# Kernel optimization log

Measured on AMD Instinct MI355X. Metric: run time of the kernel, lower is better.

Reference implementation:

```python
import jax, jax.numpy as jnp
import numpy as np
from jax import lax

EPS = 1e-5
NBIT = 127.0  # 8-bit symmetric: 2^(8-1)-1

def ste_round(x):
    return x + lax.stop_gradient(jnp.round(x) - x)

def quant_act(x, rng_max):
    # symmetric fake-quant of activations with learned per-cluster range
    s = rng_max / NBIT
    xq = jnp.clip(ste_round(x / s), -NBIT, NBIT) * s
    return xq, s

def fold_bn(w, gamma, beta, mean, var):
    std = jnp.sqrt(var + EPS)
    scale = gamma / std
    w_f = w * scale[:, None, None, None]
    b_f = beta - mean * scale
    return w_f, b_f

def quant_weight(w):
    # per-output-channel symmetric quant
    s = jnp.max(jnp.abs(w), axis=(1, 2, 3), keepdims=True) / NBIT
    wq = jnp.clip(ste_round(w / s), -NBIT, NBIT) * s
    return wq, s.reshape(-1)

def conv(x, w, stride=1, groups=1, pad=0):
    return lax.conv_general_dilated(
        x, w, window_strides=(stride, stride),
        padding=((pad, pad), (pad, pad)),
        dimension_numbers=('NCHW', 'OIHW', 'NCHW'),
        feature_group_count=groups)

def setup_inputs() -> dict:
    key = jax.random.key(0)
    ks = jax.random.split(key, 24)
    B, Cin, H, W = 64, 96, 28, 28
    Cmid, Cout, NC = 576, 96, 4
    d = {}
    d['x'] = jax.random.normal(ks[0], (B, Cin, H, W), dtype=jnp.float32)
    # conv1: 1x1 expansion
    d['w1'] = jax.random.normal(ks[1], (Cmid, Cin, 1, 1), jnp.float32) * 0.1
    d['g1'] = jax.random.uniform(ks[2], (Cmid,), minval=0.5, maxval=1.5)
    d['b1'] = jax.random.normal(ks[3], (Cmid,)) * 0.1
    d['m1'] = jax.random.normal(ks[4], (Cmid,)) * 0.1
    d['v1'] = jax.random.uniform(ks[5], (Cmid,), minval=0.5, maxval=1.5)
    # conv2: 3x3 depthwise
    d['w2'] = jax.random.normal(ks[6], (Cmid, 1, 3, 3), jnp.float32) * 0.1
    d['g2'] = jax.random.uniform(ks[7], (Cmid,), minval=0.5, maxval=1.5)
    d['b2'] = jax.random.normal(ks[8], (Cmid,)) * 0.1
    d['m2'] = jax.random.normal(ks[9], (Cmid,)) * 0.1
    d['v2'] = jax.random.uniform(ks[10], (Cmid,), minval=0.5, maxval=1.5)
    # conv3: 1x1 projection
    d['w3'] = jax.random.normal(ks[11], (Cout, Cmid, 1, 1), jnp.float32) * 0.1
    d['g3'] = jax.random.uniform(ks[12], (Cout,), minval=0.5, maxval=1.5)
    d['b3'] = jax.random.normal(ks[13], (Cout,)) * 0.1
    d['m3'] = jax.random.normal(ks[14], (Cout,)) * 0.1
    d['v3'] = jax.random.uniform(ks[15], (Cout,), minval=0.5, maxval=1.5)
    # per-cluster learned activation ranges for the 4 QuantAct modules
    d['r0'] = jax.random.uniform(ks[16], (NC,), minval=2.0, maxval=8.0)
    d['r1'] = jax.random.uniform(ks[17], (NC,), minval=2.0, maxval=8.0)
    d['r2'] = jax.random.uniform(ks[18], (NC,), minval=2.0, maxval=8.0)
    d['r3'] = jax.random.uniform(ks[19], (NC,), minval=2.0, maxval=8.0)
    d['cluster'] = 2
    return d

def reference(x, w1, g1, b1, m1, v1, w2, g2, b2, m2, v2,
              w3, g3, b3, m3, v3, r0, r1, r2, r3, cluster):
    identity = x  # residual path (in==out, stride==1)
    # QuantAct -> conv1 (BN-folded, per-channel quant) -> ReLU6
    xq, s0 = quant_act(x, r0[cluster])
    w1f, bf1 = fold_bn(w1, g1, b1, m1, v1)
    w1q, ws1 = quant_weight(w1f)
    y = conv(xq, w1q) + bf1[None, :, None, None]
    y = jnp.clip(y, 0.0, 6.0)
    # QuantAct1 -> depthwise conv2 -> ReLU6
    yq, s1 = quant_act(y, r1[cluster])
    w2f, bf2 = fold_bn(w2, g2, b2, m2, v2)
    w2q, ws2 = quant_weight(w2f)
    y = conv(yq, w2q, stride=1, groups=w2.shape[0], pad=1) + bf2[None, :, None, None]
    y = jnp.clip(y, 0.0, 6.0)
    # QuantAct2 -> conv3 projection
    yq, s2 = quant_act(y, r2[cluster])
    w3f, bf3 = fold_bn(w3, g3, b3, m3, v3)
    w3q, ws3 = quant_weight(w3f)
    y = conv(yq, w3q) + bf3[None, :, None, None]
    # residual add, then int32 requant
    y = y + identity
    out, s3 = quant_act(y, r3[cluster])
    return out, s3
```

## Files before the change

### kernel.cpp

```cpp
#include <hip/hip_runtime.h>
#include <cstdint>
#include <cstddef>

typedef int   v4i __attribute__((ext_vector_type(4)));
typedef float v4f __attribute__((ext_vector_type(4)));
typedef unsigned int u32;

constexpr int B_   = 64;
constexpr int CIN  = 96;
constexpr int P_   = 784;
constexpr int CMID = 576;
constexpr int COUT = 96;
constexpr int NOUT = B_ * COUT * P_;
constexpr float NBITF = 127.0f;
constexpr float EPSF  = 1e-5f;
constexpr float MAGICF = 12582912.0f;
constexpr int   BIASI  = 0x4B400000;

constexpr int XB4 = 13 * 8 * 64;
constexpr int YB4 = 13 * 36 * 64;

__device__ __forceinline__ int dot3(u32 a, u32 w, int acc) {
#if __has_builtin(__builtin_amdgcn_sdot4)
    return __builtin_amdgcn_sdot4((int)a, (int)w, acc, false);
#else
    return acc + (int)(signed char)(a)        * (int)(signed char)(w)
               + (int)(signed char)(a >> 8)   * (int)(signed char)(w >> 8)
               + (int)(signed char)(a >> 16)  * (int)(signed char)(w >> 16);
#endif
}

__device__ __forceinline__ void tr4(u32 S0, u32 S1, u32 S2, u32 S3, u32 O[4]) {
    u32 u01 = __builtin_amdgcn_perm(S1, S0, 0x05010400u);
    u32 u23 = __builtin_amdgcn_perm(S3, S2, 0x05010400u);
    u32 v01 = __builtin_amdgcn_perm(S1, S0, 0x07030602u);
    u32 v23 = __builtin_amdgcn_perm(S3, S2, 0x07030602u);
    O[0] = __builtin_amdgcn_perm(u23, u01, 0x05040100u);
    O[1] = __builtin_amdgcn_perm(u23, u01, 0x07060302u);
    O[2] = __builtin_amdgcn_perm(v23, v01, 0x05040100u);
    O[3] = __builtin_amdgcn_perm(v23, v01, 0x07060302u);
}

__device__ __forceinline__ u32 pack4(u32 t0, u32 t1, u32 t2, u32 t3) {
    u32 p01 = __builtin_amdgcn_perm(t1, t0, 0x05010400u);
    u32 p23 = __builtin_amdgcn_perm(t3, t2, 0x05010400u);
    return __builtin_amdgcn_perm(p23, p01, 0x05040100u);
}

__global__ __launch_bounds__(256)
void prep_all(const float* __restrict__ x,
              const float* __restrict__ w1, const float* __restrict__ g1,
              const float* __restrict__ b1, const float* __restrict__ m1,
              const float* __restrict__ v1,
              const float* __restrict__ w2, const float* __restrict__ g2,
              const float* __restrict__ b2, const float* __restrict__ m2,
              const float* __restrict__ v2,
              const float* __restrict__ w3, const float* __restrict__ g3,
              const float* __restrict__ b3, const float* __restrict__ m3,
              const float* __restrict__ v3,
              const float* __restrict__ r0, const int* __restrict__ cluster,
              u32* __restrict__ x8t2,
              int8_t* __restrict__ w1qp, float* __restrict__ ws1, float* __restrict__ bf1,
              v4i* __restrict__ w2pk, float* __restrict__ ws2, float* __restrict__ bf2,
              int8_t* __restrict__ w3qp, float* __restrict__ ws3, float* __restrict__ bf3)
{
    __shared__ u32 T[112 * 37];
    int tid = threadIdx.x;

    if (blockIdx.x < 448) {
        int pt0 = blockIdx.x % 7, b = blockIdx.x / 7;
        float inv_s0 = NBITF / r0[cluster[0]];

        for (int i = tid; i < 112 * 8; i += 256) {
            int row = i >> 3, c = 24 + (i & 7);
            T[row * 37 + c] = 0u;
        }
        for (int u = tid; u < 24 * 28; u += 256) {
            int pq = u % 28, icq = u / 28;
            int pxb = pt0 * 112 + pq * 4;
            int q[4][4];
            #pragma unroll
            for (int j = 0; j < 4; j++) {
                v4f xv = *(const v4f*)(x + ((size_t)b * CIN + icq * 4 + j) * P_ + pxb);
                #pragma unroll
                for (int i = 0; i < 4; i++)
                    q[j][i] = (int)fminf(fmaxf(rintf(xv[i] * inv_s0), -127.f), 127.f);
            }
            #pragma unroll
            for (int i = 0; i < 4; i++) {
                u32 t0 = __builtin_amdgcn_perm((u32)q[1][i], (u32)q[0][i], 0x00000400u);
                u32 t1 = __builtin_amdgcn_perm((u32)q[3][i], (u32)q[2][i], 0x00000400u);
                T[(pq * 4 + i) * 37 + icq] = __builtin_amdgcn_perm(t1, t0, 0x05040100u);
            }
        }
        __syncthreads();
        u32* gb = x8t2 + (size_t)b * XB4 * 4;
        for (int i = tid; i < 32 * 112; i += 256) {
            int icq = i / 112, pxo = i - icq * 112;
            int px = pt0 * 112 + pxo;
            gb[(((px >> 6) * 8 + (icq >> 2)) * 64 + (px & 63)) * 4 + (icq & 3)] =
                T[pxo * 37 + icq];
        }
        return;
    }

    int lane = tid & 63, wv = tid >> 6;
    int blk = (blockIdx.x - 448) * 4 + wv;

    const float *w, *g, *bb, *mm, *vv;
    int oc, K, which;
    if (blk < CMID)            { which = 0; w = w1; g = g1; bb = b1; mm = m1; vv = v1; oc = blk;            K = CIN;  }
    else if (blk < 2 * CMID)   { which = 1; w = w2; g = g2; bb = b2; mm = m2; vv = v2; oc = blk - CMID;     K = 9;    }
    else                       { which = 2; w = w3; g = g3; bb = b3; mm = m3; vv = v3; oc = blk - 2 * CMID; K = CMID; }

    float scale = g[oc] / sqrtf(vv[oc] + EPSF);

    float mx = 0.f;
    for (int k = lane; k < K; k += 64)
        mx = fmaxf(mx, fabsf(w[oc * K + k] * scale));
    #pragma unroll
    for (int off = 1; off < 64; off <<= 1)
        mx = fmaxf(mx, __shfl_xor(mx, off));

    float s = mx / NBITF;

    int myq = 0;
    for (int k = lane; k < K; k += 64) {
        float wf = w[oc * K + k] * scale;
        float q  = fminf(fmaxf(rintf(wf / s), -127.f), 127.f);
        if (which == 0)      w1qp[oc * 144 + k] = (int8_t)q;
        else if (which == 1) myq = (int)q;
        else                 w3qp[oc * 592 + k] = (int8_t)q;
    }
    if (which == 0 && lane < 12)
        ((u32*)(w1qp + oc * 144))[24 + lane] = 0u;
    if (which == 1) {
        u32 qq[9];
        #pragma unroll
        for (int t = 0; t < 9; t++) qq[t] = (u32)__shfl(myq, t, 64) & 0xffu;
        if (lane == 0) {
            v4i pk;
            pk[0] = (int)(qq[0] | (qq[1] << 8) | (qq[2] << 16));
            pk[1] = (int)(qq[3] | (qq[4] << 8) | (qq[5] << 16));
            pk[2] = (int)(qq[6] | (qq[7] << 8) | (qq[8] << 16));
            pk[3] = 0;
            w2pk[oc] = pk;
        }
    }
    if (lane == 0) {
        float bf = bb[oc] - mm[oc] * scale;
        if (which == 0)      { ws1[oc] = s; bf1[oc] = bf; }
        else if (which == 1) { ws2[oc] = s; bf2[oc] = bf; }
        else                 { ws3[oc] = s; bf3[oc] = bf; }
    }
}

__global__ __launch_bounds__(256)
void conv12r(const u32* __restrict__ x8t2, const int8_t* __restrict__ w1qp,
             const float* __restrict__ ws1, const float* __restrict__ bf1,
             const v4i* __restrict__ w2pk, const float* __restrict__ ws2,
             const float* __restrict__ bf2,
             const float* __restrict__ r0, const float* __restrict__ r1,
             const float* __restrict__ r2, const int* __restrict__ cluster,
             v4i* __restrict__ y2t)
{
    __shared__ u32 y1w[192 * 29];
    __shared__ u32 y2s[192 * 15];

    int tid = threadIdx.x, b = blockIdx.y;
    int mt = blockIdx.x / 14, rt = blockIdx.x - mt * 14;
    int R0 = 2 * rt;
    int W0 = (R0 - 1) * 28;
    int lane = tid & 63, wv = tid >> 6;
    int n = lane & 15, q4 = lane >> 4;
    int ocw = mt * 192 + wv * 48;

    int   c      = cluster[0];
    float s0     = r0[c] / NBITF;
    float s1     = r1[c] / NBITF;
    float inv_s1 = NBITF / r1[c];
    float inv_s2 = NBITF / r2[c];
    int   u1i    = (int)fminf(rintf(6.f * inv_s1), 127.f);
    int   u2i    = (int)fminf(rintf(6.f * inv_s2), 127.f);

    const v4i* xb = (const v4i*)x8t2 + (size_t)b * XB4;
    int pb[7];
    #pragma unroll
    for (int jm = 0; jm < 7; jm++) {
        int px = W0 + 16 * jm + n;
        px = min(max(px, 0), P_ - 1);
        pb[jm] = (px >> 6) * 512 + (px & 63);
    }

    v4i acc[3][7];
    #pragma unroll
    for (int jn = 0; jn < 3; jn++)
        #pragma unroll
        for (int jm = 0; jm < 7; jm++) acc[jn][jm] = (v4i){0, 0, 0, 0};

    const v4i* w4 = (const v4i*)w1qp;
    #pragma unroll
    for (int ks = 0; ks < 2; ks++) {
        v4i bw[3];
        #pragma unroll
        for (int jn = 0; jn < 3; jn++)
            bw[jn] = w4[(ocw + 16 * jn + n) * 9 + 4 * ks + q4];
        int go = (4 * ks + q4) * 64;
        #pragma unroll
        for (int jm = 0; jm < 7; jm++) {
            v4i af = xb[pb[jm] + go];
            #pragma unroll
            for (int jn = 0; jn < 3; jn++)
                acc[jn][jm] = __builtin_amdgcn_mfma_i32_16x16x64_i8(af, bw[jn], acc[jn][jm], 0, 0, 0);
        }
    }

    #pragma unroll
    for (int jn = 0; jn < 3; jn++) {
        int   oc  = ocw + 16 * jn + n;
        int   chl = wv * 48 + 16 * jn + n;
        float scv = s0 * ws1[oc] * inv_s1;
        float bbv = bf1[oc] * inv_s1;
        #pragma unroll
        for (int jm = 0; jm < 7; jm++) {
            u32 t[4];
            #pragma unroll
            for (int r = 0; r < 4; r++) {
                float f = fmaf((float)acc[jn][jm][r], scv, bbv) + MAGICF;
                t[r] = (u32)min(max(__float_as_int(f), BIASI), BIASI + u1i);
            }
            int dw = 4 * jm + q4;
            u32 pk = pack4(t[0], t[1], t[2], t[3]);
            pk = ((unsigned)(W0 + 4 * dw) < (unsigned)P_) ? pk : 0u;
            y1w[chl * 29 + dw] = pk;
        }
    }
    __syncthreads();

    for (int u = tid; u < 384; u += 256) {
        int chl = u >> 1, orow = u & 1;
        int ch  = mt * 192 + chl;
        int rb  = chl * 29 + orow * 7;

        v4i wpk = w2pk[ch];
        u32 pk0 = (u32)wpk[0], pk1 = (u32)wpk[1], pk2 = (u32)wpk[2];
        float scv = s1 * ws2[ch] * inv_s2;
        float bbv = bf2[ch] * inv_s2;

        u32 M0 = 0, M1 = 0, M2 = 0;
        u32 D0 = y1w[rb], D1 = y1w[rb + 7], D2 = y1w[rb + 14];
        #pragma unroll
        for (int xq = 0; xq < 7; xq++) {
            u32 N0, N1, N2;
            if (xq < 6) {
                N0 = y1w[rb + xq + 1];
                N1 = y1w[rb + 7 + xq + 1];
                N2 = y1w[rb + 14 + xq + 1];
            } else { N0 = N1 = N2 = 0u; }

            int a0, a1, a2, a3;
            a0 = dot3(__builtin_amdgcn_alignbyte(D0, M0, 3), pk0, 0);
            a0 = dot3(__builtin_amdgcn_alignbyte(D1, M1, 3), pk1, a0);
            a0 = dot3(__builtin_amdgcn_alignbyte(D2, M2, 3), pk2, a0);
            a1 = dot3(D0, pk0, 0);
            a1 = dot3(D1, pk1, a1);
            a1 = dot3(D2, pk2, a1);
            a2 = dot3(__builtin_amdgcn_alignbyte(N0, D0, 1), pk0, 0);
            a2 = dot3(__builtin_amdgcn_alignbyte(N1, D1, 1), pk1, a2);
            a2 = dot3(__builtin_amdgcn_alignbyte(N2, D2, 1), pk2, a2);
            a3 = dot3(__builtin_amdgcn_alignbyte(N0, D0, 2), pk0, 0);
            a3 = dot3(__builtin_amdgcn_alignbyte(N1, D1, 2), pk1, a3);
            a3 = dot3(__builtin_amdgcn_alignbyte(N2, D2, 2), pk2, a3);

            int aa[4] = {a0, a1, a2, a3};
            u32 tq[4];
            #pragma unroll
            for (int i = 0; i < 4; i++) {
                float f = fmaf((float)aa[i], scv, bbv) + MAGICF;
                tq[i] = (u32)min(max(__float_as_int(f), BIASI), BIASI + u2i);
            }
            y2s[chl * 15 + orow * 7 + xq] = pack4(tq[0], tq[1], tq[2], tq[3]);

            M0 = D0; M1 = D1; M2 = D2;
            D0 = N0; D1 = N1; D2 = N2;
        }
    }
    __syncthreads();

    v4i* yb = y2t + (size_t)b * YB4;
    for (int u = tid; u < 168; u += 256) {
        int kgl = u / 14, d = u - kgl * 14;
        u32 O[4][4];
        #pragma unroll
        for (int j = 0; j < 4; j++) {
            int cb = (16 * kgl + 4 * j) * 15 + d;
            tr4(y2s[cb], y2s[cb + 15], y2s[cb + 30], y2s[cb + 45], O[j]);
        }
        int gpx0 = R0 * 28 + 4 * d;
        #pragma unroll
        for (int i = 0; i < 4; i++) {
            int gp = gpx0 + i;
            v4i val = (v4i){(int)O[0][i], (int)O[1][i], (int)O[2][i], (int)O[3][i]};
            yb[((gp >> 6) * 36 + mt * 12 + kgl) * 64 + (gp & 63)] = val;
        }
    }
}

__global__ __launch_bounds__(256)
void conv3d(const v4i* __restrict__ y2t, const int8_t* __restrict__ w3qp,
            const float* __restrict__ ws3, const float* __restrict__ bf3,
            const float* __restrict__ x, const float* __restrict__ r2,
            const float* __restrict__ r3, const int* __restrict__ cluster,
            float* __restrict__ out)
{
    int tid = threadIdx.x, b = blockIdx.y, pt = blockIdx.x;
    int lane = tid & 63, wv = tid >> 6;
    int n = lane & 15, q4 = lane >> 4;
    int pxl = wv * 16 + n;
    int px  = pt * 64 + pxl;
    int pxc = min(px, P_ - 1);

    int   c      = cluster[0];
    float s2     = r2[c] / NBITF;
    float s3     = r3[c] / NBITF;
    float inv_s3 = NBITF / r3[c];

    const v4i* yb  = y2t + (size_t)b * YB4;
    int pb3 = (pxc >> 6) * (36 * 64) + (pxc & 63);
    const v4i* w34 = (const v4i*)w3qp;

    v4i acc[6];
    #pragma unroll
    for (int i = 0; i < 6; i++) acc[i] = (v4i){0, 0, 0, 0};

    #pragma unroll
    for (int ks = 0; ks < 9; ks++) {
        v4i bfr = yb[pb3 + (4 * ks + q4) * 64];
        #pragma unroll
        for (int i = 0; i < 6; i++) {
            v4i afr = w34[(i * 16 + n) * 37 + 4 * ks + q4];
            acc[i] = __builtin_amdgcn_mfma_i32_16x16x64_i8(afr, bfr, acc[i], 0, 0, 0);
        }
    }

    if (px < P_) {
        #pragma unroll
        for (int i = 0; i < 6; i++) {
            #pragma unroll
            for (int r = 0; r < 4; r++) {
                int oc = i * 16 + q4 * 4 + r;
                size_t gi = (size_t)(b * COUT + oc) * P_ + px;
                float v  = (float)acc[i][r] * (s2 * ws3[oc]) + bf3[oc] + x[gi];
                float f  = fmaf(v, inv_s3, MAGICF);
                int lvl  = min(max(__float_as_int(f) - BIASI, -127), 127);
                out[gi]  = (float)lvl * s3;
            }
        }
    }
    if (pt == 0 && b == 0 && tid == 0)
        out[NOUT] = s3;
}

extern "C" void kernel_launch(void* const* d_in, const int* in_sizes, int n_in,
                              void* d_out, int out_size, void* d_ws, size_t ws_size,
                              hipStream_t stream)
{
    const float* x  = (const float*)d_in[0];
    const float* w1 = (const float*)d_in[1];
    const float* g1 = (const float*)d_in[2];
    const float* b1 = (const float*)d_in[3];
    const float* m1 = (const float*)d_in[4];
    const float* v1 = (const float*)d_in[5];
    const float* w2 = (const float*)d_in[6];
    const float* g2 = (const float*)d_in[7];
    const float* b2 = (const float*)d_in[8];
    const float* m2 = (const float*)d_in[9];
    const float* v2 = (const float*)d_in[10];
    const float* w3 = (const float*)d_in[11];
    const float* g3 = (const float*)d_in[12];
    const float* b3 = (const float*)d_in[13];
    const float* m3 = (const float*)d_in[14];
    const float* v3 = (const float*)d_in[15];
    const float* r0 = (const float*)d_in[16];
    const float* r1 = (const float*)d_in[17];
    const float* r2 = (const float*)d_in[18];
    const float* r3 = (const float*)d_in[19];
    const int*   cl = (const int*)d_in[20];

    float* out = (float*)d_out;

    char*  ws  = (char*)d_ws;
    size_t off = 0;
    auto carve = [&](size_t bytes) {
        size_t cur = off;
        off = (off + bytes + 255) & ~(size_t)255;
        return (void*)(ws + cur);
    };
    int8_t* w1qp = (int8_t*)carve((size_t)CMID * 144);
    float*  ws1  = (float*)carve(CMID * 4);
    float*  bf1  = (float*)carve(CMID * 4);
    v4i*    w2pk = (v4i*)carve((size_t)CMID * 16);
    float*  ws2  = (float*)carve(CMID * 4);
    float*  bf2  = (float*)carve(CMID * 4);
    int8_t* w3qp = (int8_t*)carve((size_t)COUT * 592);
    float*  ws3  = (float*)carve(COUT * 4);
    float*  bf3  = (float*)carve(COUT * 4);
    u32*    x8t2 = (u32*)carve((size_t)B_ * XB4 * 16);
    v4i*    y2t  = (v4i*)carve((size_t)B_ * YB4 * 16);
    (void)ws_size; (void)in_sizes; (void)n_in; (void)out_size;

    prep_all<<<dim3(760), dim3(256), 0, stream>>>(
        x, w1, g1, b1, m1, v1, w2, g2, b2, m2, v2, w3, g3, b3, m3, v3,
        r0, cl, x8t2,
        w1qp, ws1, bf1, w2pk, ws2, bf2, w3qp, ws3, bf3);

    conv12r<<<dim3(42, B_), dim3(256), 0, stream>>>(
        x8t2, w1qp, ws1, bf1, w2pk, ws2, bf2, r0, r1, r2, cl, y2t);

    conv3d<<<dim3(13, B_), dim3(256), 0, stream>>>(
        y2t, w3qp, ws3, bf3, x, r2, r3, cl, out);
}
```

Baseline: 177.6 us.

## Move depthwise conv into projection kernel, materialize conv1 output globally

The fusion boundary moves: conv1 now runs as its own kernel and writes quantized int8 activations to global memory, without recomputing halo rows. A new kernel reads those rows, does the depthwise 3x3 for all 576 channels per two-row tile, transposes in shared memory and runs the projection MFMA plus residual requant, so the y2 tensor never goes to global memory. Per-channel scale and bias are also pre-folded into float2 pairs during prep. The cost is a larger global intermediate for y1 (about 29 MB) and a big LDS footprint in the fused kernel, which may reduce occupancy.

```diff
diff --git a/kernel.cpp b/kernel.cpp
--- a/kernel.cpp
+++ b/kernel.cpp
@@ -18,7 +18,6 @@
 constexpr int   BIASI  = 0x4B400000;
 
 constexpr int XB4 = 13 * 8 * 64;
-constexpr int YB4 = 13 * 36 * 64;
 
 __device__ __forceinline__ int dot3(u32 a, u32 w, int acc) {
 #if __has_builtin(__builtin_amdgcn_sdot4)
@@ -58,22 +57,24 @@
               const float* __restrict__ w3, const float* __restrict__ g3,
               const float* __restrict__ b3, const float* __restrict__ m3,
               const float* __restrict__ v3,
-              const float* __restrict__ r0, const int* __restrict__ cluster,
+              const float* __restrict__ r0, const float* __restrict__ r1,
+              const float* __restrict__ r2, const int* __restrict__ cluster,
               u32* __restrict__ x8t2,
-              int8_t* __restrict__ w1qp, float* __restrict__ ws1, float* __restrict__ bf1,
-              v4i* __restrict__ w2pk, float* __restrict__ ws2, float* __restrict__ bf2,
-              int8_t* __restrict__ w3qp, float* __restrict__ ws3, float* __restrict__ bf3)
+              int8_t* __restrict__ w1qp, float2* __restrict__ e1,
+              v4i* __restrict__ w2pk,    float2* __restrict__ e2,
+              int8_t* __restrict__ w3qp, float2* __restrict__ e3)
 {
     __shared__ u32 T[112 * 37];
     int tid = threadIdx.x;
+    int c = cluster[0];
 
     if (blockIdx.x < 448) {
         int pt0 = blockIdx.x % 7, b = blockIdx.x / 7;
-        float inv_s0 = NBITF / r0[cluster[0]];
+        float inv_s0 = NBITF / r0[c];
 
         for (int i = tid; i < 112 * 8; i += 256) {
-            int row = i >> 3, c = 24 + (i & 7);
-            T[row * 37 + c] = 0u;
+            int row = i >> 3, cc = 24 + (i & 7);
+            T[row * 37 + cc] = 0u;
         }
         for (int u = tid; u < 24 * 28; u += 256) {
             int pq = u % 28, icq = u / 28;
@@ -149,66 +150,59 @@
     }
     if (lane == 0) {
         float bf = bb[oc] - mm[oc] * scale;
-        if (which == 0)      { ws1[oc] = s; bf1[oc] = bf; }
-        else if (which == 1) { ws2[oc] = s; bf2[oc] = bf; }
-        else                 { ws3[oc] = s; bf3[oc] = bf; }
+        float s0 = r0[c] / NBITF, s1 = r1[c] / NBITF, s2 = r2[c] / NBITF;
+        if (which == 0) {
+            float inv_s1 = NBITF / r1[c];
+            e1[oc] = make_float2(s0 * s * inv_s1, bf * inv_s1);
+        } else if (which == 1) {
+            float inv_s2 = NBITF / r2[c];
+            e2[oc] = make_float2(s1 * s * inv_s2, bf * inv_s2);
+        } else {
+            e3[oc] = make_float2(s2 * s, bf);
+        }
     }
 }
 
 __global__ __launch_bounds__(256)
-void conv12r(const u32* __restrict__ x8t2, const int8_t* __restrict__ w1qp,
-             const float* __restrict__ ws1, const float* __restrict__ bf1,
-             const v4i* __restrict__ w2pk, const float* __restrict__ ws2,
-             const float* __restrict__ bf2,
-             const float* __restrict__ r0, const float* __restrict__ r1,
-             const float* __restrict__ r2, const int* __restrict__ cluster,
-             v4i* __restrict__ y2t)
+void conv1f(const v4i* __restrict__ x8t2, const v4i* __restrict__ w1q4,
+            const float2* __restrict__ e1, const float* __restrict__ r1,
+            const int* __restrict__ cluster, u32* __restrict__ y1px)
 {
-    __shared__ u32 y1w[192 * 29];
-    __shared__ u32 y2s[192 * 15];
+    __shared__ u32 L[192 * 20];
 
     int tid = threadIdx.x, b = blockIdx.y;
-    int mt = blockIdx.x / 14, rt = blockIdx.x - mt * 14;
-    int R0 = 2 * rt;
-    int W0 = (R0 - 1) * 28;
+    int mt = blockIdx.x % 3, pt = blockIdx.x / 3;
+    int p0 = pt * 64;
     int lane = tid & 63, wv = tid >> 6;
     int n = lane & 15, q4 = lane >> 4;
     int ocw = mt * 192 + wv * 48;
 
-    int   c      = cluster[0];
-    float s0     = r0[c] / NBITF;
-    float s1     = r1[c] / NBITF;
-    float inv_s1 = NBITF / r1[c];
-    float inv_s2 = NBITF / r2[c];
-    int   u1i    = (int)fminf(rintf(6.f * inv_s1), 127.f);
-    int   u2i    = (int)fminf(rintf(6.f * inv_s2), 127.f);
-
-    const v4i* xb = (const v4i*)x8t2 + (size_t)b * XB4;
-    int pb[7];
-    #pragma unroll
-    for (int jm = 0; jm < 7; jm++) {
-        int px = W0 + 16 * jm + n;
-        px = min(max(px, 0), P_ - 1);
+    int u1i = (int)fminf(rintf(6.f * NBITF / r1[cluster[0]]), 127.f);
+
+    const v4i* xb = x8t2 + (size_t)b * XB4;
+    int pb[4];
+    #pragma unroll
+    for (int jm = 0; jm < 4; jm++) {
+        int px = min(p0 + 16 * jm + n, P_ - 1);
         pb[jm] = (px >> 6) * 512 + (px & 63);
     }
 
-    v4i acc[3][7];
+    v4i acc[3][4];
     #pragma unroll
     for (int jn = 0; jn < 3; jn++)
         #pragma unroll
-        for (int jm = 0; jm < 7; jm++) acc[jn][jm] = (v4i){0, 0, 0, 0};
-
-    const v4i* w4 = (const v4i*)w1qp;
+        for (int jm = 0; jm < 4; jm++) acc[jn][jm] = (v4i){0, 0, 0, 0};
+
     #pragma unroll
     for (int ks = 0; ks < 2; ks++) {
+        int g = 4 * ks + q4;
         v4i bw[3];
         #pragma unroll
         for (int jn = 0; jn < 3; jn++)
-            bw[jn] = w4[(ocw + 16 * jn + n) * 9 + 4 * ks + q4];
-        int go = (4 * ks + q4) * 64;
-        #pragma unroll
-        for (int jm = 0; jm < 7; jm++) {
-            v4i af = xb[pb[jm] + go];
+            bw[jn] = w1q4[(ocw + 16 * jn + n) * 9 + g];
+        #pragma unroll
+        for (int jm = 0; jm < 4; jm++) {
+            v4i af = xb[pb[jm] + g * 64];
             #pragma unroll
             for (int jn = 0; jn < 3; jn++)
                 acc[jn][jm] = __builtin_amdgcn_mfma_i32_16x16x64_i8(af, bw[jn], acc[jn][jm], 0, 0, 0);
@@ -217,116 +211,127 @@
 
     #pragma unroll
     for (int jn = 0; jn < 3; jn++) {
-        int   oc  = ocw + 16 * jn + n;
-        int   chl = wv * 48 + 16 * jn + n;
-        float scv = s0 * ws1[oc] * inv_s1;
-        float bbv = bf1[oc] * inv_s1;
-        #pragma unroll
-        for (int jm = 0; jm < 7; jm++) {
+        int    ocl = wv * 48 + 16 * jn + n;
+        float2 e   = e1[ocw + 16 * jn + n];
+        #pragma unroll
+        for (int jm = 0; jm < 4; jm++) {
             u32 t[4];
             #pragma unroll
             for (int r = 0; r < 4; r++) {
-                float f = fmaf((float)acc[jn][jm][r], scv, bbv) + MAGICF;
+                float f = fmaf((float)acc[jn][jm][r], e.x, e.y) + MAGICF;
                 t[r] = (u32)min(max(__float_as_int(f), BIASI), BIASI + u1i);
             }
-            int dw = 4 * jm + q4;
-            u32 pk = pack4(t[0], t[1], t[2], t[3]);
-            pk = ((unsigned)(W0 + 4 * dw) < (unsigned)P_) ? pk : 0u;
-            y1w[chl * 29 + dw] = pk;
+            L[ocl * 20 + 4 * jm + q4] = pack4(t[0], t[1], t[2], t[3]);
         }
     }
     __syncthreads();
 
-    for (int u = tid; u < 384; u += 256) {
-        int chl = u >> 1, orow = u & 1;
-        int ch  = mt * 192 + chl;
-        int rb  = chl * 29 + orow * 7;
-
+    for (int u = tid; u < 768; u += 256) {
+        int ocl = u >> 2, dq = u & 3;
+        int dwg = pt * 16 + 4 * dq;
+        if (dwg < 196) {
+            v4i val = *(const v4i*)&L[ocl * 20 + 4 * dq];
+            *(v4i*)&y1px[(size_t)(b * CMID + mt * 192 + ocl) * 196 + dwg] = val;
+        }
+    }
+}
+
+__global__ __launch_bounds__(256)
+void conv23f(const u32* __restrict__ y1px, const v4i* __restrict__ w2pk,
+             const float2* __restrict__ e2, const int8_t* __restrict__ w3qp,
+             const float2* __restrict__ e3, const float* __restrict__ x,
+             const float* __restrict__ r2, const float* __restrict__ r3,
+             const int* __restrict__ cluster, float* __restrict__ out)
+{
+    __shared__ u32 y2px[CMID * 15];
+    __shared__ v4i y2t[36 * 57];
+
+    int tid = threadIdx.x, b = blockIdx.y, rt = blockIdx.x;
+    int R0 = 2 * rt;
+
+    int   c      = cluster[0];
+    float inv_s3 = NBITF / r3[c];
+    float s3     = r3[c] / NBITF;
+    int   u2i    = (int)fminf(rintf(6.f * NBITF / r2[c]), 127.f);
+
+    for (int ch = tid; ch < CMID; ch += 256) {
+        const u32* base = y1px + (size_t)(b * CMID + ch) * 196;
+        u32 row[4][7];
+        #pragma unroll
+        for (int j = 0; j < 4; j++) {
+            int rr = R0 - 1 + j;
+            bool ok = (unsigned)rr < 28u;
+            #pragma unroll
+            for (int k = 0; k < 7; k++)
+                row[j][k] = ok ? base[rr * 7 + k] : 0u;
+        }
         v4i wpk = w2pk[ch];
         u32 pk0 = (u32)wpk[0], pk1 = (u32)wpk[1], pk2 = (u32)wpk[2];
-        float scv = s1 * ws2[ch] * inv_s2;
-        float bbv = bf2[ch] * inv_s2;
-
-        u32 M0 = 0, M1 = 0, M2 = 0;
-        u32 D0 = y1w[rb], D1 = y1w[rb + 7], D2 = y1w[rb + 14];
-        #pragma unroll
-        for (int xq = 0; xq < 7; xq++) {
-            u32 N0, N1, N2;
-            if (xq < 6) {
-                N0 = y1w[rb + xq + 1];
-                N1 = y1w[rb + 7 + xq + 1];
-                N2 = y1w[rb + 14 + xq + 1];
-            } else { N0 = N1 = N2 = 0u; }
-
-            int a0, a1, a2, a3;
-            a0 = dot3(__builtin_amdgcn_alignbyte(D0, M0, 3), pk0, 0);
-            a0 = dot3(__builtin_amdgcn_alignbyte(D1, M1, 3), pk1, a0);
-            a0 = dot3(__builtin_amdgcn_alignbyte(D2, M2, 3), pk2, a0);
-            a1 = dot3(D0, pk0, 0);
-            a1 = dot3(D1, pk1, a1);
-            a1 = dot3(D2, pk2, a1);
-            a2 = dot3(__builtin_amdgcn_alignbyte(N0, D0, 1), pk0, 0);
-            a2 = dot3(__builtin_amdgcn_alignbyte(N1, D1, 1), pk1, a2);
-            a2 = dot3(__builtin_amdgcn_alignbyte(N2, D2, 1), pk2, a2);
-            a3 = dot3(__builtin_amdgcn_alignbyte(N0, D0, 2), pk0, 0);
-            a3 = dot3(__builtin_amdgcn_alignbyte(N1, D1, 2), pk1, a3);
-            a3 = dot3(__builtin_amdgcn_alignbyte(N2, D2, 2), pk2, a3);
-
-            int aa[4] = {a0, a1, a2, a3};
-            u32 tq[4];
-            #pragma unroll
-            for (int i = 0; i < 4; i++) {
-                float f = fmaf((float)aa[i], scv, bbv) + MAGICF;
-                tq[i] = (u32)min(max(__float_as_int(f), BIASI), BIASI + u2i);
+        float2 e = e2[ch];
+
+        #pragma unroll
+        for (int orow = 0; orow < 2; orow++) {
+            u32 M0 = 0, M1 = 0, M2 = 0;
+            u32 D0 = row[orow][0], D1 = row[orow + 1][0], D2 = row[orow + 2][0];
+            #pragma unroll
+            for (int xq = 0; xq < 7; xq++) {
+                u32 N0, N1, N2;
+                if (xq < 6) {
+                    N0 = row[orow][xq + 1];
+                    N1 = row[orow + 1][xq + 1];
+                    N2 = row[orow + 2][xq + 1];
+                } else { N0 = N1 = N2 = 0u; }
+
+                int a0, a1, a2, a3;
+                a0 = dot3(__builtin_amdgcn_alignbyte(D0, M0, 3), pk0, 0);
+                a0 = dot3(__builtin_amdgcn_alignbyte(D1, M1, 3), pk1, a0);
+                a0 = dot3(__builtin_amdgcn_alignbyte(D2, M2, 3), pk2, a0);
+                a1 = dot3(D0, pk0, 0);
+                a1 = dot3(D1, pk1, a1);
+                a1 = dot3(D2, pk2, a1);
+                a2 = dot3(__builtin_amdgcn_alignbyte(N0, D0, 1), pk0, 0);
+                a2 = dot3(__builtin_amdgcn_alignbyte(N1, D1, 1), pk1, a2);
+                a2 = dot3(__builtin_amdgcn_alignbyte(N2, D2, 1), pk2, a2);
+                a3 = dot3(__builtin_amdgcn_alignbyte(N0, D0, 2), pk0, 0);
+                a3 = dot3(__builtin_amdgcn_alignbyte(N1, D1, 2), pk1, a3);
+                a3 = dot3(__builtin_amdgcn_alignbyte(N2, D2, 2), pk2, a3);
+
+                int aa[4] = {a0, a1, a2, a3};
+                u32 tq[4];
+                #pragma unroll
+                for (int i = 0; i < 4; i++) {
+                    float f = fmaf((float)aa[i], e.x, e.y) + MAGICF;
+                    tq[i] = (u32)min(max(__float_as_int(f), BIASI), BIASI + u2i);
+                }
+                y2px[ch * 15 + orow * 7 + xq] = pack4(tq[0], tq[1], tq[2], tq[3]);
+
+                M0 = D0; M1 = D1; M2 = D2;
+                D0 = N0; D1 = N1; D2 = N2;
             }
-            y2s[chl * 15 + orow * 7 + xq] = pack4(tq[0], tq[1], tq[2], tq[3]);
-
-            M0 = D0; M1 = D1; M2 = D2;
-            D0 = N0; D1 = N1; D2 = N2;
         }
     }
     __syncthreads();
 
-    v4i* yb = y2t + (size_t)b * YB4;
-    for (int u = tid; u < 168; u += 256) {
-        int kgl = u / 14, d = u - kgl * 14;
+    for (int u = tid; u < 504; u += 256) {
+        int kg = u / 14, d = u - kg * 14;
         u32 O[4][4];
         #pragma unroll
         for (int j = 0; j < 4; j++) {
-            int cb = (16 * kgl + 4 * j) * 15 + d;
-            tr4(y2s[cb], y2s[cb + 15], y2s[cb + 30], y2s[cb + 45], O[j]);
-        }
-        int gpx0 = R0 * 28 + 4 * d;
-        #pragma unroll
-        for (int i = 0; i < 4; i++) {
-            int gp = gpx0 + i;
-            v4i val = (v4i){(int)O[0][i], (int)O[1][i], (int)O[2][i], (int)O[3][i]};
-            yb[((gp >> 6) * 36 + mt * 12 + kgl) * 64 + (gp & 63)] = val;
-        }
-    }
-}
-
-__global__ __launch_bounds__(256)
-void conv3d(const v4i* __restrict__ y2t, const int8_t* __restrict__ w3qp,
-            const float* __restrict__ ws3, const float* __restrict__ bf3,
-            const float* __restrict__ x, const float* __restrict__ r2,
-            const float* __restrict__ r3, const int* __restrict__ cluster,
-            float* __restrict__ out)
-{
-    int tid = threadIdx.x, b = blockIdx.y, pt = blockIdx.x;
+            int cb = (16 * kg + 4 * j) * 15 + d;
+            tr4(y2px[cb], y2px[cb + 15], y2px[cb + 30], y2px[cb + 45], O[j]);
+        }
+        #pragma unroll
+        for (int i = 0; i < 4; i++)
+            y2t[kg * 57 + 4 * d + i] =
+                (v4i){(int)O[0][i], (int)O[1][i], (int)O[2][i], (int)O[3][i]};
+    }
+    __syncthreads();
+
     int lane = tid & 63, wv = tid >> 6;
     int n = lane & 15, q4 = lane >> 4;
     int pxl = wv * 16 + n;
-    int px  = pt * 64 + pxl;
-    int pxc = min(px, P_ - 1);
-
-    int   c      = cluster[0];
-    float s2     = r2[c] / NBITF;
-    float s3     = r3[c] / NBITF;
-    float inv_s3 = NBITF / r3[c];
-
-    const v4i* yb  = y2t + (size_t)b * YB4;
-    int pb3 = (pxc >> 6) * (36 * 64) + (pxc & 63);
+    int pxc = min(pxl, 55);
+
     const v4i* w34 = (const v4i*)w3qp;
 
     v4i acc[6];
@@ -335,7 +340,7 @@
 
     #pragma unroll
     for (int ks = 0; ks < 9; ks++) {
-        v4i bfr = yb[pb3 + (4 * ks + q4) * 64];
+        v4i bfr = y2t[(4 * ks + q4) * 57 + pxc];
         #pragma unroll
         for (int i = 0; i < 6; i++) {
             v4i afr = w34[(i * 16 + n) * 37 + 4 * ks + q4];
@@ -343,21 +348,23 @@
         }
     }
 
-    if (px < P_) {
+    if (pxl < 56) {
+        int px = R0 * 28 + pxl;
         #pragma unroll
         for (int i = 0; i < 6; i++) {
             #pragma unroll
             for (int r = 0; r < 4; r++) {
-                int oc = i * 16 + q4 * 4 + r;
+                int    oc = i * 16 + q4 * 4 + r;
+                float2 e  = e3[oc];
                 size_t gi = (size_t)(b * COUT + oc) * P_ + px;
-                float v  = (float)acc[i][r] * (s2 * ws3[oc]) + bf3[oc] + x[gi];
+                float v  = fmaf((float)acc[i][r], e.x, e.y) + x[gi];
                 float f  = fmaf(v, inv_s3, MAGICF);
                 int lvl  = min(max(__float_as_int(f) - BIASI, -127), 127);
                 out[gi]  = (float)lvl * s3;
             }
         }
     }
-    if (pt == 0 && b == 0 && tid == 0)
+    if (rt == 0 && b == 0 && tid == 0)
         out[NOUT] = s3;
 }
 
@@ -397,26 +404,23 @@
         return (void*)(ws + cur);
     };
     int8_t* w1qp = (int8_t*)carve((size_t)CMID * 144);
-    float*  ws1  = (float*)carve(CMID * 4);
-    float*  bf1  = (float*)carve(CMID * 4);
+    float2* e1   = (float2*)carve((size_t)CMID * 8);
     v4i*    w2pk = (v4i*)carve((size_t)CMID * 16);
-    float*  ws2  = (float*)carve(CMID * 4);
-    float*  bf2  = (float*)carve(CMID * 4);
+    float2* e2   = (float2*)carve((size_t)CMID * 8);
     int8_t* w3qp = (int8_t*)carve((size_t)COUT * 592);
-    float*  ws3  = (float*)carve(COUT * 4);
-    float*  bf3  = (float*)carve(COUT * 4);
+    float2* e3   = (float2*)carve((size_t)COUT * 8);
     u32*    x8t2 = (u32*)carve((size_t)B_ * XB4 * 16);
-    v4i*    y2t  = (v4i*)carve((size_t)B_ * YB4 * 16);
+    u32*    y1px = (u32*)carve((size_t)B_ * CMID * 196 * 4);
     (void)ws_size; (void)in_sizes; (void)n_in; (void)out_size;
 
     prep_all<<<dim3(760), dim3(256), 0, stream>>>(
         x, w1, g1, b1, m1, v1, w2, g2, b2, m2, v2, w3, g3, b3, m3, v3,
-        r0, cl, x8t2,
-        w1qp, ws1, bf1, w2pk, ws2, bf2, w3qp, ws3, bf3);
-
-    conv12r<<<dim3(42, B_), dim3(256), 0, stream>>>(
-        x8t2, w1qp, ws1, bf1, w2pk, ws2, bf2, r0, r1, r2, cl, y2t);
-
-    conv3d<<<dim3(13, B_), dim3(256), 0, stream>>>(
-        y2t, w3qp, ws3, bf3, x, r2, r3, cl, out);
-}
+        r0, r1, r2, cl, x8t2,
+        w1qp, e1, w2pk, e2, w3qp, e3);
+
+    conv1f<<<dim3(39, B_), dim3(256), 0, stream>>>(
+        (const v4i*)x8t2, (const v4i*)w1qp, e1, r1, cl, y1px);
+
+    conv23f<<<dim3(14, B_), dim3(256), 0, stream>>>(
+        y1px, w2pk, e2, w3qp, e3, x, r2, r3, cl, out);
+}
```

Result: slower. 199.2 us (+12.1%).

## Stage input tile in LDS for conv1 and precompute fused per-channel epilogue scales

Applied to the files above, without the earlier changes.

conv12 now loads the int8 input tile for its 112 pixels into shared memory once, instead of every wave reading the fragments from global memory, and the shared pool is reused afterward for the depthwise output. The jn loop is moved outside, so each wave keeps only 7 accumulators at a time rather than 21, which lowers register pressure. The requant scale and bias for each channel are now computed once in prep_all and stored as float2, so the conv kernels read one pair instead of recombining several scalars. The cost is an extra __syncthreads and an LDS staging pass at the start of conv12.

```diff
diff --git a/kernel.cpp b/kernel.cpp
--- a/kernel.cpp
+++ b/kernel.cpp
@@ -58,22 +58,24 @@
               const float* __restrict__ w3, const float* __restrict__ g3,
               const float* __restrict__ b3, const float* __restrict__ m3,
               const float* __restrict__ v3,
-              const float* __restrict__ r0, const int* __restrict__ cluster,
+              const float* __restrict__ r0, const float* __restrict__ r1,
+              const float* __restrict__ r2, const int* __restrict__ cluster,
               u32* __restrict__ x8t2,
-              int8_t* __restrict__ w1qp, float* __restrict__ ws1, float* __restrict__ bf1,
-              v4i* __restrict__ w2pk, float* __restrict__ ws2, float* __restrict__ bf2,
-              int8_t* __restrict__ w3qp, float* __restrict__ ws3, float* __restrict__ bf3)
+              int8_t* __restrict__ w1qp, float2* __restrict__ e1,
+              v4i* __restrict__ w2pk,    float2* __restrict__ e2,
+              int8_t* __restrict__ w3qp, float2* __restrict__ e3)
 {
     __shared__ u32 T[112 * 37];
     int tid = threadIdx.x;
+    int c = cluster[0];
 
     if (blockIdx.x < 448) {
         int pt0 = blockIdx.x % 7, b = blockIdx.x / 7;
-        float inv_s0 = NBITF / r0[cluster[0]];
+        float inv_s0 = NBITF / r0[c];
 
         for (int i = tid; i < 112 * 8; i += 256) {
-            int row = i >> 3, c = 24 + (i & 7);
-            T[row * 37 + c] = 0u;
+            int row = i >> 3, cc = 24 + (i & 7);
+            T[row * 37 + cc] = 0u;
         }
         for (int u = tid; u < 24 * 28; u += 256) {
             int pq = u % 28, icq = u / 28;
@@ -149,23 +151,28 @@
     }
     if (lane == 0) {
         float bf = bb[oc] - mm[oc] * scale;
-        if (which == 0)      { ws1[oc] = s; bf1[oc] = bf; }
-        else if (which == 1) { ws2[oc] = s; bf2[oc] = bf; }
-        else                 { ws3[oc] = s; bf3[oc] = bf; }
+        float s0 = r0[c] / NBITF, s1 = r1[c] / NBITF, s2 = r2[c] / NBITF;
+        if (which == 0) {
+            float inv_s1 = NBITF / r1[c];
+            e1[oc] = make_float2(s0 * s * inv_s1, bf * inv_s1);
+        } else if (which == 1) {
+            float inv_s2 = NBITF / r2[c];
+            e2[oc] = make_float2(s1 * s * inv_s2, bf * inv_s2);
+        } else {
+            e3[oc] = make_float2(s2 * s, bf);
+        }
     }
 }
 
 __global__ __launch_bounds__(256)
-void conv12r(const u32* __restrict__ x8t2, const int8_t* __restrict__ w1qp,
-             const float* __restrict__ ws1, const float* __restrict__ bf1,
-             const v4i* __restrict__ w2pk, const float* __restrict__ ws2,
-             const float* __restrict__ bf2,
-             const float* __restrict__ r0, const float* __restrict__ r1,
-             const float* __restrict__ r2, const int* __restrict__ cluster,
-             v4i* __restrict__ y2t)
+void conv12v3(const v4i* __restrict__ x8t2, const v4i* __restrict__ w1q4,
+              const float2* __restrict__ e1,
+              const v4i* __restrict__ w2pk, const float2* __restrict__ e2,
+              const float* __restrict__ r1, const float* __restrict__ r2,
+              const int* __restrict__ cluster, v4i* __restrict__ y2t)
 {
+    __shared__ u32 pool[112 * 36];
     __shared__ u32 y1w[192 * 29];
-    __shared__ u32 y2s[192 * 15];
 
     int tid = threadIdx.x, b = blockIdx.y;
     int mt = blockIdx.x / 14, rt = blockIdx.x - mt * 14;
@@ -175,58 +182,46 @@
     int n = lane & 15, q4 = lane >> 4;
     int ocw = mt * 192 + wv * 48;
 
-    int   c      = cluster[0];
-    float s0     = r0[c] / NBITF;
-    float s1     = r1[c] / NBITF;
-    float inv_s1 = NBITF / r1[c];
-    float inv_s2 = NBITF / r2[c];
-    int   u1i    = (int)fminf(rintf(6.f * inv_s1), 127.f);
-    int   u2i    = (int)fminf(rintf(6.f * inv_s2), 127.f);
-
-    const v4i* xb = (const v4i*)x8t2 + (size_t)b * XB4;
-    int pb[7];
-    #pragma unroll
-    for (int jm = 0; jm < 7; jm++) {
-        int px = W0 + 16 * jm + n;
-        px = min(max(px, 0), P_ - 1);
-        pb[jm] = (px >> 6) * 512 + (px & 63);
-    }
-
-    v4i acc[3][7];
-    #pragma unroll
-    for (int jn = 0; jn < 3; jn++)
-        #pragma unroll
-        for (int jm = 0; jm < 7; jm++) acc[jn][jm] = (v4i){0, 0, 0, 0};
-
-    const v4i* w4 = (const v4i*)w1qp;
-    #pragma unroll
-    for (int ks = 0; ks < 2; ks++) {
-        v4i bw[3];
-        #pragma unroll
-        for (int jn = 0; jn < 3; jn++)
-            bw[jn] = w4[(ocw + 16 * jn + n) * 9 + 4 * ks + q4];
-        int go = (4 * ks + q4) * 64;
-        #pragma unroll
-        for (int jm = 0; jm < 7; jm++) {
-            v4i af = xb[pb[jm] + go];
-            #pragma unroll
-            for (int jn = 0; jn < 3; jn++)
-                acc[jn][jm] = __builtin_amdgcn_mfma_i32_16x16x64_i8(af, bw[jn], acc[jn][jm], 0, 0, 0);
-        }
-    }
+    int c   = cluster[0];
+    int u1i = (int)fminf(rintf(6.f * NBITF / r1[c]), 127.f);
+    int u2i = (int)fminf(rintf(6.f * NBITF / r2[c]), 127.f);
+
+    const v4i* xb = x8t2 + (size_t)b * XB4;
+    for (int u = tid; u < 896; u += 256) {
+        int g = u / 112, pxl = u - g * 112;
+        int px = min(max(W0 + pxl, 0), P_ - 1);
+        v4i v = xb[((px >> 6) * 8 + g) * 64 + (px & 63)];
+        *(v4i*)&pool[pxl * 36 + 4 * g] = v;
+    }
+    __syncthreads();
 
     #pragma unroll
     for (int jn = 0; jn < 3; jn++) {
-        int   oc  = ocw + 16 * jn + n;
-        int   chl = wv * 48 + 16 * jn + n;
-        float scv = s0 * ws1[oc] * inv_s1;
-        float bbv = bf1[oc] * inv_s1;
+        int oc  = ocw + 16 * jn + n;
+        int chl = wv * 48 + 16 * jn + n;
+
+        v4i acc[7];
+        #pragma unroll
+        for (int jm = 0; jm < 7; jm++) acc[jm] = (v4i){0, 0, 0, 0};
+
+        #pragma unroll
+        for (int ks = 0; ks < 2; ks++) {
+            v4i bw = w1q4[oc * 9 + 4 * ks + q4];
+            int g4 = (4 * ks + q4) * 4;
+            #pragma unroll
+            for (int jm = 0; jm < 7; jm++) {
+                v4i af = *(const v4i*)&pool[(16 * jm + n) * 36 + g4];
+                acc[jm] = __builtin_amdgcn_mfma_i32_16x16x64_i8(af, bw, acc[jm], 0, 0, 0);
+            }
+        }
+
+        float2 e = e1[oc];
         #pragma unroll
         for (int jm = 0; jm < 7; jm++) {
             u32 t[4];
             #pragma unroll
             for (int r = 0; r < 4; r++) {
-                float f = fmaf((float)acc[jn][jm][r], scv, bbv) + MAGICF;
+                float f = fmaf((float)acc[jm][r], e.x, e.y) + MAGICF;
                 t[r] = (u32)min(max(__float_as_int(f), BIASI), BIASI + u1i);
             }
             int dw = 4 * jm + q4;
@@ -237,6 +232,7 @@
     }
     __syncthreads();
 
+    u32* y2s = pool;
     for (int u = tid; u < 384; u += 256) {
         int chl = u >> 1, orow = u & 1;
         int ch  = mt * 192 + chl;
@@ -244,8 +240,7 @@
 
         v4i wpk = w2pk[ch];
         u32 pk0 = (u32)wpk[0], pk1 = (u32)wpk[1], pk2 = (u32)wpk[2];
-        float scv = s1 * ws2[ch] * inv_s2;
-        float bbv = bf2[ch] * inv_s2;
+        float2 e = e2[ch];
 
         u32 M0 = 0, M1 = 0, M2 = 0;
         u32 D0 = y1w[rb], D1 = y1w[rb + 7], D2 = y1w[rb + 14];
@@ -276,7 +271,7 @@
             u32 tq[4];
             #pragma unroll
             for (int i = 0; i < 4; i++) {
-                float f = fmaf((float)aa[i], scv, bbv) + MAGICF;
+                float f = fmaf((float)aa[i], e.x, e.y) + MAGICF;
                 tq[i] = (u32)min(max(__float_as_int(f), BIASI), BIASI + u2i);
             }
             y2s[chl * 15 + orow * 7 + xq] = pack4(tq[0], tq[1], tq[2], tq[3]);
@@ -308,8 +303,7 @@
 
 __global__ __launch_bounds__(256)
 void conv3d(const v4i* __restrict__ y2t, const int8_t* __restrict__ w3qp,
-            const float* __restrict__ ws3, const float* __restrict__ bf3,
-            const float* __restrict__ x, const float* __restrict__ r2,
+            const float2* __restrict__ e3, const float* __restrict__ x,
             const float* __restrict__ r3, const int* __restrict__ cluster,
             float* __restrict__ out)
 {
@@ -321,7 +315,6 @@
     int pxc = min(px, P_ - 1);
 
     int   c      = cluster[0];
-    float s2     = r2[c] / NBITF;
     float s3     = r3[c] / NBITF;
     float inv_s3 = NBITF / r3[c];
 
@@ -348,9 +341,10 @@
         for (int i = 0; i < 6; i++) {
             #pragma unroll
             for (int r = 0; r < 4; r++) {
-                int oc = i * 16 + q4 * 4 + r;
+                int    oc = i * 16 + q4 * 4 + r;
+                float2 e  = e3[oc];
                 size_t gi = (size_t)(b * COUT + oc) * P_ + px;
-                float v  = (float)acc[i][r] * (s2 * ws3[oc]) + bf3[oc] + x[gi];
+                float v  = fmaf((float)acc[i][r], e.x, e.y) + x[gi];
                 float f  = fmaf(v, inv_s3, MAGICF);
                 int lvl  = min(max(__float_as_int(f) - BIASI, -127), 127);
                 out[gi]  = (float)lvl * s3;
@@ -397,26 +391,23 @@
         return (void*)(ws + cur);
     };
     int8_t* w1qp = (int8_t*)carve((size_t)CMID * 144);
-    float*  ws1  = (float*)carve(CMID * 4);
-    float*  bf1  = (float*)carve(CMID * 4);
+    float2* e1   = (float2*)carve((size_t)CMID * 8);
     v4i*    w2pk = (v4i*)carve((size_t)CMID * 16);
-    float*  ws2  = (float*)carve(CMID * 4);
-    float*  bf2  = (float*)carve(CMID * 4);
+    float2* e2   = (float2*)carve((size_t)CMID * 8);
     int8_t* w3qp = (int8_t*)carve((size_t)COUT * 592);
-    float*  ws3  = (float*)carve(COUT * 4);
-    float*  bf3  = (float*)carve(COUT * 4);
+    float2* e3   = (float2*)carve((size_t)COUT * 8);
     u32*    x8t2 = (u32*)carve((size_t)B_ * XB4 * 16);
     v4i*    y2t  = (v4i*)carve((size_t)B_ * YB4 * 16);
     (void)ws_size; (void)in_sizes; (void)n_in; (void)out_size;
 
     prep_all<<<dim3(760), dim3(256), 0, stream>>>(
         x, w1, g1, b1, m1, v1, w2, g2, b2, m2, v2, w3, g3, b3, m3, v3,
-        r0, cl, x8t2,
-        w1qp, ws1, bf1, w2pk, ws2, bf2, w3qp, ws3, bf3);
-
-    conv12r<<<dim3(42, B_), dim3(256), 0, stream>>>(
-        x8t2, w1qp, ws1, bf1, w2pk, ws2, bf2, r0, r1, r2, cl, y2t);
+        r0, r1, r2, cl, x8t2,
+        w1qp, e1, w2pk, e2, w3qp, e3);
+
+    conv12v3<<<dim3(42, B_), dim3(256), 0, stream>>>(
+        (const v4i*)x8t2, (const v4i*)w1qp, e1, w2pk, e2, r1, r2, cl, y2t);
 
     conv3d<<<dim3(13, B_), dim3(256), 0, stream>>>(
-        y2t, w3qp, ws3, bf3, x, r2, r3, cl, out);
-}
+        y2t, w3qp, e3, x, r3, cl, out);
+}
```

Result: no change. 174.7 us (-1.6%).
